# Kernel optimization log

Hardware: AMD Instinct MI355X
Metric: run time of the kernel (lower is better)

## Reference

```python
import jax, jax.numpy as jnp
import numpy as np

HEADS = 8
DIM_HEAD = 64


def setup_inputs() -> dict:
    key = jax.random.key(0)
    ks = jax.random.split(key, 6)
    dim = 512
    inner = HEADS * DIM_HEAD  # 512
    x = jax.random.normal(ks[0], (4, 4096, dim), dtype=jnp.float32)
    s = 1.0 / np.sqrt(dim)
    Wq = jax.random.normal(ks[1], (dim, inner), dtype=jnp.float32) * s
    Wk = jax.random.normal(ks[2], (dim, inner), dtype=jnp.float32) * s
    Wv = jax.random.normal(ks[3], (dim, inner), dtype=jnp.float32) * s
    Wo = jax.random.normal(ks[4], (inner, dim), dtype=jnp.float32) * (1.0 / np.sqrt(inner))
    bo = jax.random.normal(ks[5], (dim,), dtype=jnp.float32) * 0.01
    return {"x": x, "Wq": Wq, "Wk": Wk, "Wv": Wv, "Wo": Wo, "bo": bo}


def reference(x, Wq, Wk, Wv, Wo, bo):
    b, n, _ = x.shape
    h, d = HEADS, DIM_HEAD
    # project and split heads: [b, h, n, d]
    q = (x @ Wq).reshape(b, n, h, d).transpose(0, 2, 1, 3)
    k = (x @ Wk).reshape(b, n, h, d).transpose(0, 2, 1, 3)
    v = (x @ Wv).reshape(b, n, h, d).transpose(0, 2, 1, 3)
    q = jax.nn.softmax(q, axis=-1)
    k = jax.nn.softmax(k, axis=-1)
    context = jnp.einsum('bhnd,bhne->bhde', k, v)  # small d x d per head
    out = jnp.einsum('bhnd,bhde->bhne', q, context)
    out = out.transpose(0, 2, 1, 3).reshape(b, n, h * d)
    return out @ Wo + bo
```

## Files before the change

### kernel.cpp

```cpp
#include <hip/hip_runtime.h>

typedef unsigned short u16;
typedef unsigned int   u32;
typedef __bf16 bf16x8 __attribute__((ext_vector_type(8)));
typedef float  f32x4  __attribute__((ext_vector_type(4)));
typedef u16    u16x8  __attribute__((ext_vector_type(8)));
typedef u16    u16x4  __attribute__((ext_vector_type(4)));

__device__ __forceinline__ float b2f(u16 h) {
  return __builtin_bit_cast(float, ((u32)h) << 16);
}
__device__ __forceinline__ u16 f2b(float f) {
  u32 u = __builtin_bit_cast(u32, f);
  u32 r = u + 0x7FFFu + ((u >> 16) & 1u);
  return (u16)(r >> 16);
}

#define GLD_AS1(p) ((const __attribute__((address_space(1))) void*)(p))
#define LDS_AS3(p) ((__attribute__((address_space(3))) void*)(p))

__global__ void gemm_qkv_kernel(const u16* __restrict__ A, const u16* __restrict__ Bt,
                                u16* __restrict__ qb, float* __restrict__ ctxp) {
  const int K = 512;
  __shared__ u16 smem[24576];
  const int id = blockIdx.x;
  const int tn = id >> 7;
  const int tm = (id & 7) * 16 + ((id >> 3) & 15);
  const int tileM = tm * 128;
  const int t = threadIdx.x;
  const int lane = t & 63;
  const int wave = t >> 6;
  const int mbase = (wave >> 1) * 64;
  const int nbase = (wave & 1) * 64;
  const int fm = lane & 15;
  const int kg = lane >> 4;
  const bool is_q = (tn < 4);
  const int j = tn - 4;

  f32x4 acc[4][4];
#pragma unroll
  for (int i = 0; i < 4; ++i)
#pragma unroll
    for (int jj = 0; jj < 4; ++jj) acc[i][jj] = (f32x4){0.f, 0.f, 0.f, 0.f};

  auto stage = [&](int buf, int k0) {
    u16* As = smem + buf * 8192;
    u16* Bs = As + 4096;
#pragma unroll
    for (int p = 0; p < 2; ++p) {
      int c = p * 256 + t;
      int r = c >> 2;
      int g = (c & 3) ^ ((r >> 1) & 3);
      const u16* ga = A + (size_t)(tileM + r) * K + (k0 + g * 8);
      __builtin_amdgcn_global_load_lds(GLD_AS1(ga), LDS_AS3(As + c * 8), 16, 0, 0);
      int brow = is_q ? (tn * 128 + r) : (512 + j * 64 + r + (r >> 6) * 448);
      const u16* gb = Bt + (size_t)brow * K + (k0 + g * 8);
      __builtin_amdgcn_global_load_lds(GLD_AS1(gb), LDS_AS3(Bs + c * 8), 16, 0, 0);
    }
  };

  stage(0, 0);
  stage(1, 32);
  stage(2, 64);

  int cur = 0;
  for (int kk = 0; kk < 16; ++kk) {
    if (kk <= 13)      asm volatile("s_waitcnt vmcnt(8)" ::: "memory");
    else if (kk == 14) asm volatile("s_waitcnt vmcnt(4)" ::: "memory");
    else               asm volatile("s_waitcnt vmcnt(0)" ::: "memory");
    __builtin_amdgcn_s_barrier();

    const u16* As = smem + cur * 8192;
    const u16* Bs = As + 4096;
    bf16x8 af[4], bfr[4];
#pragma unroll
    for (int mi = 0; mi < 4; ++mi) {
      int m = mbase + mi * 16 + fm;
      int sg = kg ^ ((m >> 1) & 3);
      af[mi] = *(const bf16x8*)(As + m * 32 + sg * 8);
    }
#pragma unroll
    for (int ni = 0; ni < 4; ++ni) {
      int n = nbase + ni * 16 + fm;
      int sg = kg ^ ((n >> 1) & 3);
      bfr[ni] = *(const bf16x8*)(Bs + n * 32 + sg * 8);
    }
    asm volatile("s_waitcnt lgkmcnt(0)" ::: "memory");
    __builtin_amdgcn_sched_barrier(0);
    __builtin_amdgcn_s_barrier();

    if (kk <= 12) stage(cur, (kk + 3) * 32);

#pragma unroll
    for (int mi = 0; mi < 4; ++mi)
#pragma unroll
      for (int ni = 0; ni < 4; ++ni)
        acc[mi][ni] = __builtin_amdgcn_mfma_f32_16x16x32_bf16(af[mi], bfr[ni],
                                                              acc[mi][ni], 0, 0, 0);
    cur = (cur == 2) ? 0 : cur + 1;
  }

  const int rq = lane >> 4;

  float inv[4][4];
  const bool do_sm = is_q || ((wave & 1) == 0);
  if (do_sm) {
#pragma unroll
    for (int mi = 0; mi < 4; ++mi)
#pragma unroll
      for (int ni = 0; ni < 4; ++ni)
#pragma unroll
        for (int reg = 0; reg < 4; ++reg)
          acc[mi][ni][reg] = __expf(acc[mi][ni][reg]);
#pragma unroll
    for (int mi = 0; mi < 4; ++mi)
#pragma unroll
      for (int reg = 0; reg < 4; ++reg) {
        float s = acc[mi][0][reg] + acc[mi][1][reg] + acc[mi][2][reg] + acc[mi][3][reg];
        s += __shfl_xor(s, 1);
        s += __shfl_xor(s, 2);
        s += __shfl_xor(s, 4);
        s += __shfl_xor(s, 8);
        inv[mi][reg] = 1.f / s;
      }
  } else {
#pragma unroll
    for (int mi = 0; mi < 4; ++mi)
#pragma unroll
      for (int reg = 0; reg < 4; ++reg) inv[mi][reg] = 1.f;
  }

  if (is_q) {
#pragma unroll
    for (int mi = 0; mi < 4; ++mi)
#pragma unroll
      for (int ni = 0; ni < 4; ++ni)
#pragma unroll
        for (int reg = 0; reg < 4; ++reg) {
          int gr = tileM + mbase + mi * 16 + rq * 4 + reg;
          int gc = tn * 128 + nbase + ni * 16 + fm;
          qb[(size_t)gr * 512 + gc] = f2b(acc[mi][ni][reg] * inv[mi][reg]);
        }
    return;
  }

  u16* T = smem;
  f32x4 cacc[4];
#pragma unroll
  for (int i = 0; i < 4; ++i) cacc[i] = (f32x4){0.f, 0.f, 0.f, 0.f};

#pragma unroll
  for (int ph = 0; ph < 2; ++ph) {
    if ((wave >> 1) == ph) {
#pragma unroll
      for (int mi = 0; mi < 4; ++mi)
#pragma unroll
        for (int ni = 0; ni < 4; ++ni) {
          u16x4 o;
#pragma unroll
          for (int reg = 0; reg < 4; ++reg)
            o[reg] = f2b(acc[mi][ni][reg] * inv[mi][reg]);
          int c = nbase + ni * 16 + fm;
          *(u16x4*)(T + c * 72 + mi * 16 + rq * 4) = o;
        }
    }
    __syncthreads();
#pragma unroll
    for (int kk = 0; kk < 2; ++kk) {
      bf16x8 afc = *(const bf16x8*)(T + (wave * 16 + fm) * 72 + kk * 32 + kg * 8);
#pragma unroll
      for (int et = 0; et < 4; ++et) {
        bf16x8 bfc = *(const bf16x8*)(T + (64 + et * 16 + fm) * 72 + kk * 32 + kg * 8);
        cacc[et] = __builtin_amdgcn_mfma_f32_16x16x32_bf16(afc, bfc, cacc[et], 0, 0, 0);
      }
    }
    __syncthreads();
  }

  const int b = tm >> 5;
  const int s = tm & 31;
  float* cp = ctxp + ((size_t)s * 32 + b * 8 + j) * 4096;
#pragma unroll
  for (int et = 0; et < 4; ++et)
#pragma unroll
    for (int reg = 0; reg < 4; ++reg)
      cp[(wave * 16 + rq * 4 + reg) * 64 + et * 16 + fm] = cacc[et][reg];
}

__global__ void prep_all_kernel(const float* __restrict__ x, const float* __restrict__ Wq,
                                const float* __restrict__ Wk, const float* __restrict__ Wv,
                                const float* __restrict__ Wo, u16* __restrict__ xb,
                                u16* __restrict__ Wt, u16* __restrict__ Wot) {
  __shared__ u16 tr[64 * 72];
  const int id = blockIdx.x;
  const int t = threadIdx.x;

  if (id < 4096) {
    int i = (id * 256 + t) * 8;
    float4 a = *(const float4*)(x + i);
    float4 b = *(const float4*)(x + i + 4);
    u16x8 o;
    o[0] = f2b(a.x); o[1] = f2b(a.y); o[2] = f2b(a.z); o[3] = f2b(a.w);
    o[4] = f2b(b.x); o[5] = f2b(b.y); o[6] = f2b(b.z); o[7] = f2b(b.w);
    *(u16x8*)(xb + i) = o;
    return;
  }
  const float* W;
  u16* dst;
  int n0, k0;
  if (id < 4288) {
    int tile = id - 4096;
    n0 = (tile >> 3) * 64;
    k0 = (tile & 7) * 64;
    W = (n0 < 512) ? Wq : ((n0 < 1024) ? Wk : Wv);
    dst = Wt;
  } else {
    int tile = id - 4288;
    n0 = (tile >> 3) * 64;
    k0 = (tile & 7) * 64;
    W = Wo;
    dst = Wot;
  }
  int cin = (n0 & 511);
  int c = t & 63;
  int r0 = t >> 6;
#pragma unroll
  for (int i = 0; i < 16; ++i) {
    int r = r0 * 16 + i;
    tr[c * 72 + r] = f2b(W[(size_t)(k0 + r) * 512 + cin + c]);
  }
  __syncthreads();
#pragma unroll
  for (int jj = 0; jj < 2; ++jj) {
    int idx = jj * 256 + t;
    int row = idx >> 3;
    int seg = idx & 7;
    u16x8 val = *(const u16x8*)(tr + row * 72 + seg * 8);
    *(u16x8*)(dst + (size_t)(n0 + row) * 512 + k0 + seg * 8) = val;
  }
}

__global__ void ctx_reduce_kernel(const float* __restrict__ ctxp, u16* __restrict__ ctxb) {
  const int id = blockIdx.x;
  const int bh = id >> 2;
  const int chunk = id & 3;
  const int t = threadIdx.x;
  const int idx = chunk * 1024 + t * 4;
  f32x4 s = (f32x4){0.f, 0.f, 0.f, 0.f};
#pragma unroll
  for (int p = 0; p < 32; ++p)
    s += *(const f32x4*)(ctxp + ((size_t)p * 32 + bh) * 4096 + idx);
  u16x4 o;
#pragma unroll
  for (int jj = 0; jj < 4; ++jj) o[jj] = f2b(s[jj]);
  *(u16x4*)(ctxb + (size_t)bh * 4096 + idx) = o;
}

__global__ void ctxm_kernel(const u16* __restrict__ ctxb, const u16* __restrict__ Wot,
                            u16* __restrict__ Mt) {
  __shared__ u16 ctxd[64 * 72];
  const int id = blockIdx.x;
  const int bh = id >> 2;
  const int cq = id & 3;
  const int b = bh >> 3, h = bh & 7;
  const int t = threadIdx.x;
  const int lane = t & 63;
  const int wave = t >> 6;
  const int fm = lane & 15;
  const int kg = lane >> 4;
  const int rq = lane >> 4;

  {
    int base = t * 16;
    int d = base >> 6, e = base & 63;
    u16x8 v0 = *(const u16x8*)(ctxb + (size_t)bh * 4096 + base);
    u16x8 v1 = *(const u16x8*)(ctxb + (size_t)bh * 4096 + base + 8);
    *(u16x8*)(ctxd + d * 72 + e) = v0;
    *(u16x8*)(ctxd + d * 72 + e + 8) = v1;
  }
  __syncthreads();

  f32x4 acc[2][4];
#pragma unroll
  for (int i = 0; i < 2; ++i)
#pragma unroll
    for (int jj = 0; jj < 4; ++jj) acc[i][jj] = (f32x4){0.f, 0.f, 0.f, 0.f};

#pragma unroll
  for (int ks = 0; ks < 2; ++ks) {
    bf16x8 bfr[4];
#pragma unroll
    for (int dt = 0; dt < 4; ++dt)
      bfr[dt] = *(const bf16x8*)(ctxd + (dt * 16 + fm) * 72 + ks * 32 + kg * 8);
#pragma unroll
    for (int mi = 0; mi < 2; ++mi) {
      int c = cq * 128 + wave * 32 + mi * 16 + fm;
      bf16x8 af = *(const bf16x8*)(Wot + (size_t)c * 512 + h * 64 + ks * 32 + kg * 8);
#pragma unroll
      for (int dt = 0; dt < 4; ++dt)
        acc[mi][dt] = __builtin_amdgcn_mfma_f32_16x16x32_bf16(af, bfr[dt],
                                                              acc[mi][dt], 0, 0, 0);
    }
  }

  u16* mb = Mt + (size_t)b * 512 * 512;
#pragma unroll
  for (int mi = 0; mi < 2; ++mi)
#pragma unroll
    for (int dt = 0; dt < 4; ++dt)
#pragma unroll
      for (int reg = 0; reg < 4; ++reg) {
        int c = cq * 128 + wave * 32 + mi * 16 + rq * 4 + reg;
        mb[(size_t)c * 512 + h * 64 + dt * 16 + fm] = f2b(acc[mi][dt][reg]);
      }
}

__global__ void gemm_out_kernel(const u16* __restrict__ A, const u16* __restrict__ Mt,
                                float* __restrict__ Cout, const float* __restrict__ bias) {
  const int K = 512, N = 512;
  __shared__ u16 smem[18432];
  const int id = blockIdx.x;
  const int tn = id >> 8;
  const int tm = (id & 7) * 32 + ((id >> 3) & 31);
  const int tileN = tn * 128;
  const int tileM = tm * 64;
  const u16* Bt = Mt + (size_t)(tm >> 6) * 512 * 512;
  const int t = threadIdx.x;
  const int lane = t & 63;
  const int wave = t >> 6;
  const int mbase = (wave >> 1) * 32;
  const int nbase = (wave & 1) * 64;
  const int fm = lane & 15;
  const int kg = lane >> 4;

  f32x4 acc[2][4];
#pragma unroll
  for (int i = 0; i < 2; ++i)
#pragma unroll
    for (int jj = 0; jj < 4; ++jj) acc[i][jj] = (f32x4){0.f, 0.f, 0.f, 0.f};

  auto stage = [&](int buf, int k0) {
    u16* As = smem + buf * 6144;
    u16* Bs = As + 2048;
    {
      int c = t;
      int r = c >> 2;
      int g = (c & 3) ^ ((r >> 1) & 3);
      const u16* ga = A + (size_t)(tileM + r) * K + (k0 + g * 8);
      __builtin_amdgcn_global_load_lds(GLD_AS1(ga), LDS_AS3(As + c * 8), 16, 0, 0);
    }
#pragma unroll
    for (int p = 0; p < 2; ++p) {
      int c = p * 256 + t;
      int r = c >> 2;
      int g = (c & 3) ^ ((r >> 1) & 3);
      const u16* gb = Bt + (size_t)(tileN + r) * K + (k0 + g * 8);
      __builtin_amdgcn_global_load_lds(GLD_AS1(gb), LDS_AS3(Bs + c * 8), 16, 0, 0);
    }
  };

  stage(0, 0);
  stage(1, 32);
  stage(2, 64);

  int cur = 0;
  for (int kk = 0; kk < 16; ++kk) {
    if (kk <= 13)      asm volatile("s_waitcnt vmcnt(6)" ::: "memory");
    else if (kk == 14) asm volatile("s_waitcnt vmcnt(3)" ::: "memory");
    else               asm volatile("s_waitcnt vmcnt(0)" ::: "memory");
    __builtin_amdgcn_s_barrier();

    const u16* As = smem + cur * 6144;
    const u16* Bs = As + 2048;
    bf16x8 af[2], bfr[4];
#pragma unroll
    for (int mi = 0; mi < 2; ++mi) {
      int m = mbase + mi * 16 + fm;
      int sg = kg ^ ((m >> 1) & 3);
      af[mi] = *(const bf16x8*)(As + m * 32 + sg * 8);
    }
#pragma unroll
    for (int ni = 0; ni < 4; ++ni) {
      int n = nbase + ni * 16 + fm;
      int sg = kg ^ ((n >> 1) & 3);
      bfr[ni] = *(const bf16x8*)(Bs + n * 32 + sg * 8);
    }
    asm volatile("s_waitcnt lgkmcnt(0)" ::: "memory");
    __builtin_amdgcn_sched_barrier(0);
    __builtin_amdgcn_s_barrier();

    if (kk <= 12) stage(cur, (kk + 3) * 32);

#pragma unroll
    for (int mi = 0; mi < 2; ++mi)
#pragma unroll
      for (int ni = 0; ni < 4; ++ni)
        acc[mi][ni] = __builtin_amdgcn_mfma_f32_16x16x32_bf16(af[mi], bfr[ni],
                                                              acc[mi][ni], 0, 0, 0);
    cur = (cur == 2) ? 0 : cur + 1;
  }

  const int rq = lane >> 4;
#pragma unroll
  for (int mi = 0; mi < 2; ++mi)
#pragma unroll
    for (int ni = 0; ni < 4; ++ni)
#pragma unroll
      for (int reg = 0; reg < 4; ++reg) {
        int gr = tileM + mbase + mi * 16 + rq * 4 + reg;
        int gc = tileN + nbase + ni * 16 + fm;
        Cout[(size_t)gr * N + gc] = acc[mi][ni][reg] + bias[gc];
      }
}

extern "C" void kernel_launch(void* const* d_in, const int* in_sizes, int n_in,
                              void* d_out, int out_size, void* d_ws, size_t ws_size,
                              hipStream_t stream) {
  const float* x  = (const float*)d_in[0];
  const float* Wq = (const float*)d_in[1];
  const float* Wk = (const float*)d_in[2];
  const float* Wv = (const float*)d_in[3];
  const float* Wo = (const float*)d_in[4];
  const float* bo = (const float*)d_in[5];

  char* w = (char*)d_ws;
  u16* xb   = (u16*)w;    w += (size_t)16384 * 512 * 2;
  u16* Wt   = (u16*)w;    w += (size_t)1536 * 512 * 2;
  u16* Wot  = (u16*)w;    w += (size_t)512 * 512 * 2;
  u16* qbuf = (u16*)w;    w += (size_t)16384 * 512 * 2;
  float* ctxp = (float*)w; w += (size_t)32 * 32 * 4096 * 4;
  u16* ctxb = (u16*)w;    w += (size_t)32 * 4096 * 2;
  u16* Mt   = (u16*)w;    w += (size_t)4 * 512 * 512 * 2;

  prep_all_kernel<<<4352, 256, 0, stream>>>(x, Wq, Wk, Wv, Wo, xb, Wt, Wot);
  gemm_qkv_kernel<<<1536, 256, 0, stream>>>(xb, Wt, qbuf, ctxp);
  ctx_reduce_kernel<<<128, 256, 0, stream>>>(ctxp, ctxb);
  ctxm_kernel<<<128, 256, 0, stream>>>(ctxb, Wot, Mt);
  gemm_out_kernel<<<1024, 256, 0, stream>>>(qbuf, Mt, (float*)d_out, bo);
}
```

Measured before the change: 154.0 us.

## Widen QKV GEMM tile to 128x256 and halve grid size

The QKV projection kernel now computes 128x256 output tiles instead of 128x128. Each wave owns a 64x128 sub-tile, so each block reuses its staged A tile across twice as many columns and the grid shrinks from 1536 to 768 blocks. The K/V epilogue now handles two heads per block and accumulates two context matrices in sequential phases. The cost is more accumulator registers (128 floats per thread) and more LDS per block (72 KB), with launch bounds set to target two blocks per CU, which may lower occupancy or cause spills.

```diff
diff --git a/kernel.cpp b/kernel.cpp
--- a/kernel.cpp
+++ b/kernel.cpp
@@ -19,32 +19,33 @@
 #define GLD_AS1(p) ((const __attribute__((address_space(1))) void*)(p))
 #define LDS_AS3(p) ((__attribute__((address_space(3))) void*)(p))
 
-__global__ void gemm_qkv_kernel(const u16* __restrict__ A, const u16* __restrict__ Bt,
-                                u16* __restrict__ qb, float* __restrict__ ctxp) {
+__global__ __launch_bounds__(256, 2)
+void gemm_qkv_kernel(const u16* __restrict__ A, const u16* __restrict__ Bt,
+                     u16* __restrict__ qb, float* __restrict__ ctxp) {
   const int K = 512;
-  __shared__ u16 smem[24576];
+  __shared__ u16 smem[36864];
   const int id = blockIdx.x;
-  const int tn = id >> 7;
+  const int tnp = id >> 7;
   const int tm = (id & 7) * 16 + ((id >> 3) & 15);
   const int tileM = tm * 128;
   const int t = threadIdx.x;
   const int lane = t & 63;
   const int wave = t >> 6;
-  const int mbase = (wave >> 1) * 64;
-  const int nbase = (wave & 1) * 64;
+  const int rbase = (wave & 1) * 64;
+  const int nbase = (wave >> 1) * 128;
   const int fm = lane & 15;
   const int kg = lane >> 4;
-  const bool is_q = (tn < 4);
-  const int j = tn - 4;
-
-  f32x4 acc[4][4];
+  const int rq = lane >> 4;
+  const bool is_q = (tnp < 2);
+
+  f32x4 acc[4][8];
 #pragma unroll
   for (int i = 0; i < 4; ++i)
 #pragma unroll
-    for (int jj = 0; jj < 4; ++jj) acc[i][jj] = (f32x4){0.f, 0.f, 0.f, 0.f};
+    for (int jj = 0; jj < 8; ++jj) acc[i][jj] = (f32x4){0.f, 0.f, 0.f, 0.f};
 
   auto stage = [&](int buf, int k0) {
-    u16* As = smem + buf * 8192;
+    u16* As = smem + buf * 12288;
     u16* Bs = As + 4096;
 #pragma unroll
     for (int p = 0; p < 2; ++p) {
@@ -53,7 +54,20 @@
       int g = (c & 3) ^ ((r >> 1) & 3);
       const u16* ga = A + (size_t)(tileM + r) * K + (k0 + g * 8);
       __builtin_amdgcn_global_load_lds(GLD_AS1(ga), LDS_AS3(As + c * 8), 16, 0, 0);
-      int brow = is_q ? (tn * 128 + r) : (512 + j * 64 + r + (r >> 6) * 448);
+    }
+#pragma unroll
+    for (int p = 0; p < 4; ++p) {
+      int c = p * 256 + t;
+      int r = c >> 2;
+      int g = (c & 3) ^ ((r >> 1) & 3);
+      int brow;
+      if (is_q) {
+        brow = tnp * 256 + r;
+      } else {
+        int jglob = (tnp - 2) * 2 + (r >> 7);
+        int r7 = r & 127;
+        brow = 512 + jglob * 64 + r7 + ((r7 >> 6) * 448);
+      }
       const u16* gb = Bt + (size_t)brow * K + (k0 + g * 8);
       __builtin_amdgcn_global_load_lds(GLD_AS1(gb), LDS_AS3(Bs + c * 8), 16, 0, 0);
     }
@@ -65,22 +79,22 @@
 
   int cur = 0;
   for (int kk = 0; kk < 16; ++kk) {
-    if (kk <= 13)      asm volatile("s_waitcnt vmcnt(8)" ::: "memory");
-    else if (kk == 14) asm volatile("s_waitcnt vmcnt(4)" ::: "memory");
+    if (kk <= 13)      asm volatile("s_waitcnt vmcnt(12)" ::: "memory");
+    else if (kk == 14) asm volatile("s_waitcnt vmcnt(6)" ::: "memory");
     else               asm volatile("s_waitcnt vmcnt(0)" ::: "memory");
     __builtin_amdgcn_s_barrier();
 
-    const u16* As = smem + cur * 8192;
+    const u16* As = smem + cur * 12288;
     const u16* Bs = As + 4096;
-    bf16x8 af[4], bfr[4];
+    bf16x8 af[4], bfr[8];
 #pragma unroll
     for (int mi = 0; mi < 4; ++mi) {
-      int m = mbase + mi * 16 + fm;
+      int m = rbase + mi * 16 + fm;
       int sg = kg ^ ((m >> 1) & 3);
       af[mi] = *(const bf16x8*)(As + m * 32 + sg * 8);
     }
 #pragma unroll
-    for (int ni = 0; ni < 4; ++ni) {
+    for (int ni = 0; ni < 8; ++ni) {
       int n = nbase + ni * 16 + fm;
       int sg = kg ^ ((n >> 1) & 3);
       bfr[ni] = *(const bf16x8*)(Bs + n * 32 + sg * 8);
@@ -94,97 +108,109 @@
 #pragma unroll
     for (int mi = 0; mi < 4; ++mi)
 #pragma unroll
-      for (int ni = 0; ni < 4; ++ni)
+      for (int ni = 0; ni < 8; ++ni)
         acc[mi][ni] = __builtin_amdgcn_mfma_f32_16x16x32_bf16(af[mi], bfr[ni],
                                                               acc[mi][ni], 0, 0, 0);
     cur = (cur == 2) ? 0 : cur + 1;
   }
 
-  const int rq = lane >> 4;
-
-  float inv[4][4];
-  const bool do_sm = is_q || ((wave & 1) == 0);
-  if (do_sm) {
+  float inv[4][2][4];
+#pragma unroll
+  for (int g = 0; g < 2; ++g) {
+    const bool sm = is_q || (g == 0);
+    if (sm) {
+#pragma unroll
+      for (int mi = 0; mi < 4; ++mi)
+#pragma unroll
+        for (int ni = g * 4; ni < g * 4 + 4; ++ni)
+#pragma unroll
+          for (int reg = 0; reg < 4; ++reg)
+            acc[mi][ni][reg] = __expf(acc[mi][ni][reg]);
+#pragma unroll
+      for (int mi = 0; mi < 4; ++mi)
+#pragma unroll
+        for (int reg = 0; reg < 4; ++reg) {
+          float s = acc[mi][g * 4 + 0][reg] + acc[mi][g * 4 + 1][reg] +
+                    acc[mi][g * 4 + 2][reg] + acc[mi][g * 4 + 3][reg];
+          s += __shfl_xor(s, 1);
+          s += __shfl_xor(s, 2);
+          s += __shfl_xor(s, 4);
+          s += __shfl_xor(s, 8);
+          inv[mi][g][reg] = 1.f / s;
+        }
+    } else {
+#pragma unroll
+      for (int mi = 0; mi < 4; ++mi)
+#pragma unroll
+        for (int reg = 0; reg < 4; ++reg) inv[mi][g][reg] = 1.f;
+    }
+  }
+
+  if (is_q) {
 #pragma unroll
     for (int mi = 0; mi < 4; ++mi)
 #pragma unroll
-      for (int ni = 0; ni < 4; ++ni)
-#pragma unroll
-        for (int reg = 0; reg < 4; ++reg)
-          acc[mi][ni][reg] = __expf(acc[mi][ni][reg]);
-#pragma unroll
-    for (int mi = 0; mi < 4; ++mi)
-#pragma unroll
-      for (int reg = 0; reg < 4; ++reg) {
-        float s = acc[mi][0][reg] + acc[mi][1][reg] + acc[mi][2][reg] + acc[mi][3][reg];
-        s += __shfl_xor(s, 1);
-        s += __shfl_xor(s, 2);
-        s += __shfl_xor(s, 4);
-        s += __shfl_xor(s, 8);
-        inv[mi][reg] = 1.f / s;
-      }
-  } else {
-#pragma unroll
-    for (int mi = 0; mi < 4; ++mi)
-#pragma unroll
-      for (int reg = 0; reg < 4; ++reg) inv[mi][reg] = 1.f;
-  }
-
-  if (is_q) {
-#pragma unroll
-    for (int mi = 0; mi < 4; ++mi)
-#pragma unroll
-      for (int ni = 0; ni < 4; ++ni)
+      for (int ni = 0; ni < 8; ++ni)
 #pragma unroll
         for (int reg = 0; reg < 4; ++reg) {
-          int gr = tileM + mbase + mi * 16 + rq * 4 + reg;
-          int gc = tn * 128 + nbase + ni * 16 + fm;
-          qb[(size_t)gr * 512 + gc] = f2b(acc[mi][ni][reg] * inv[mi][reg]);
+          int gr = tileM + rbase + mi * 16 + rq * 4 + reg;
+          int gc = tnp * 256 + nbase + ni * 16 + fm;
+          qb[(size_t)gr * 512 + gc] = f2b(acc[mi][ni][reg] * inv[mi][ni >> 2][reg]);
         }
     return;
   }
 
   u16* T = smem;
-  f32x4 cacc[4];
-#pragma unroll
-  for (int i = 0; i < 4; ++i) cacc[i] = (f32x4){0.f, 0.f, 0.f, 0.f};
-
-#pragma unroll
-  for (int ph = 0; ph < 2; ++ph) {
-    if ((wave >> 1) == ph) {
-#pragma unroll
-      for (int mi = 0; mi < 4; ++mi)
-#pragma unroll
-        for (int ni = 0; ni < 4; ++ni) {
-          u16x4 o;
-#pragma unroll
-          for (int reg = 0; reg < 4; ++reg)
-            o[reg] = f2b(acc[mi][ni][reg] * inv[mi][reg]);
-          int c = nbase + ni * 16 + fm;
-          *(u16x4*)(T + c * 72 + mi * 16 + rq * 4) = o;
+  f32x4 cacc[2][4];
+#pragma unroll
+  for (int i = 0; i < 2; ++i)
+#pragma unroll
+    for (int jj = 0; jj < 4; ++jj) cacc[i][jj] = (f32x4){0.f, 0.f, 0.f, 0.f};
+
+#pragma unroll
+  for (int jh = 0; jh < 2; ++jh) {
+#pragma unroll
+    for (int ph = 0; ph < 2; ++ph) {
+      if ((wave >> 1) == jh && (wave & 1) == ph) {
+#pragma unroll
+        for (int mi = 0; mi < 4; ++mi)
+#pragma unroll
+          for (int ni = 0; ni < 8; ++ni) {
+            u16x4 o;
+#pragma unroll
+            for (int reg = 0; reg < 4; ++reg)
+              o[reg] = f2b(acc[mi][ni][reg] * inv[mi][ni >> 2][reg]);
+            int c = ni * 16 + fm;
+            *(u16x4*)(T + c * 72 + mi * 16 + rq * 4) = o;
+          }
+      }
+      __syncthreads();
+#pragma unroll
+      for (int kc = 0; kc < 2; ++kc) {
+        bf16x8 afc = *(const bf16x8*)(T + (wave * 16 + fm) * 72 + kc * 32 + kg * 8);
+#pragma unroll
+        for (int et = 0; et < 4; ++et) {
+          bf16x8 bfc = *(const bf16x8*)(T + (64 + et * 16 + fm) * 72 + kc * 32 + kg * 8);
+          cacc[jh][et] = __builtin_amdgcn_mfma_f32_16x16x32_bf16(afc, bfc,
+                                                                 cacc[jh][et], 0, 0, 0);
         }
-    }
-    __syncthreads();
-#pragma unroll
-    for (int kk = 0; kk < 2; ++kk) {
-      bf16x8 afc = *(const bf16x8*)(T + (wave * 16 + fm) * 72 + kk * 32 + kg * 8);
-#pragma unroll
-      for (int et = 0; et < 4; ++et) {
-        bf16x8 bfc = *(const bf16x8*)(T + (64 + et * 16 + fm) * 72 + kk * 32 + kg * 8);
-        cacc[et] = __builtin_amdgcn_mfma_f32_16x16x32_bf16(afc, bfc, cacc[et], 0, 0, 0);
       }
-    }
-    __syncthreads();
+      __syncthreads();
+    }
   }
 
   const int b = tm >> 5;
   const int s = tm & 31;
-  float* cp = ctxp + ((size_t)s * 32 + b * 8 + j) * 4096;
-#pragma unroll
-  for (int et = 0; et < 4; ++et)
-#pragma unroll
-    for (int reg = 0; reg < 4; ++reg)
-      cp[(wave * 16 + rq * 4 + reg) * 64 + et * 16 + fm] = cacc[et][reg];
+#pragma unroll
+  for (int jh = 0; jh < 2; ++jh) {
+    int jglob = (tnp - 2) * 2 + jh;
+    float* cp = ctxp + ((size_t)s * 32 + b * 8 + jglob) * 4096;
+#pragma unroll
+    for (int et = 0; et < 4; ++et)
+#pragma unroll
+      for (int reg = 0; reg < 4; ++reg)
+        cp[(wave * 16 + rq * 4 + reg) * 64 + et * 16 + fm] = cacc[jh][et][reg];
+  }
 }
 
 __global__ void prep_all_kernel(const float* __restrict__ x, const float* __restrict__ Wq,
@@ -433,7 +459,7 @@
   u16* Mt   = (u16*)w;    w += (size_t)4 * 512 * 512 * 2;
 
   prep_all_kernel<<<4352, 256, 0, stream>>>(x, Wq, Wk, Wv, Wo, xb, Wt, Wot);
-  gemm_qkv_kernel<<<1536, 256, 0, stream>>>(xb, Wt, qbuf, ctxp);
+  gemm_qkv_kernel<<<768, 256, 0, stream>>>(xb, Wt, qbuf, ctxp);
   ctx_reduce_kernel<<<128, 256, 0, stream>>>(ctxp, ctxb);
   ctxm_kernel<<<128, 256, 0, stream>>>(ctxb, Wot, Mt);
   gemm_out_kernel<<<1024, 256, 0, stream>>>(qbuf, Mt, (float*)d_out, bo);
```

Result: slower. 214.3 us (+39.2%).
